# Performance work log

Hardware: AMD Instinct MI355X
Metric: run time of the kernel (lower is better)

Reference implementation:

```python
import jax, jax.numpy as jnp
import numpy as np

# dims (match init_kwargs)
N, M = 128, 2048
DX, DY, DU, DZ = 64, 8, 256, 256
EPS = 0.01


def setup_inputs() -> dict:
    key = jax.random.key(0)
    kit = iter(jax.random.split(key, 40))
    def w(*shape):
        fan_in = shape[-1]
        return jax.random.normal(next(kit), shape, jnp.float32) / np.float32(np.sqrt(fan_in))
    def b(*shape):
        return 0.1 * jax.random.normal(next(kit), shape, jnp.float32)
    inp = {
        'X_tensor': jax.random.normal(next(kit), (N, DX), jnp.float32),
        'U_tensor': jax.random.normal(next(kit), (M, DY), jnp.float32),
        'Y_tensor': jax.random.normal(next(kit), (N, DY), jnp.float32),
        # context path (x -> u_i)
        'Wt0': w(DU, DX), 'bt0': b(DU),
        'Wt1': w(DU, DU), 'bt1': b(DU),
        # PICNN cell 0 (input cell, no z term)
        'Wyu0': w(DY, DX), 'byu0': b(DY), 'Wy0': w(DZ, DY), 'Wu0': w(DZ, DX), 'b0': b(DZ),
        # PICNN cell 1 (hidden cell, nonneg Wz1 via softplus)
        'Wzu1': w(DZ, DU), 'bzu1': b(DZ), 'Wz1': w(DZ, DZ),
        'Wyu1': w(DY, DU), 'byu1': b(DY), 'Wy1': w(DZ, DY), 'Wu1': w(DZ, DU), 'b1': b(DZ),
        # PICNN cell 2 (output cell, scalar potential)
        'Wzu2': w(DZ, DU), 'bzu2': b(DZ), 'Wz2': w(1, DZ),
        'Wyu2': w(DY, DU), 'byu2': b(DY), 'Wy2': w(1, DY), 'Wu2': w(1, DU), 'b2': b(1),
    }
    return inp


def _psi(X, U, Y, Wt0, bt0, Wt1, bt1, Wyu0, byu0, Wy0, Wu0, b0,
         Wzu1, bzu1, Wz1, Wyu1, byu1, Wy1, Wu1, b1,
         Wzu2, bzu2, Wz2, Wyu2, byu2, Wy2, Wu2, b2):
    relu = jax.nn.relu
    # context path depends only on X -> compute once per row, broadcast over m samples
    u1 = relu(X @ Wt0.T + bt0)                       # [n, du]
    u2 = relu(u1 @ Wt1.T + bt1)                      # [n, du]
    # cell 0: z1 [n, m, dz]  (pairwise over X rows x U samples)
    gy0 = X @ Wyu0.T + byu0                          # [n, dy]
    z1 = relu(jnp.einsum('md,nd,zd->nmz', U, gy0, Wy0)
              + (X @ Wu0.T + b0)[:, None, :])
    # cell 1: hidden convex cell with nonneg z-weight
    gz1 = relu(u1 @ Wzu1.T + bzu1)                   # [n, dz]
    gy1 = u1 @ Wyu1.T + byu1                         # [n, dy]
    z2 = relu(jnp.einsum('nmz,nz,kz->nmk', z1, gz1, jax.nn.softplus(Wz1))
              + jnp.einsum('md,nd,kd->nmk', U, gy1, Wy1)
              + (u1 @ Wu1.T + b1)[:, None, :])       # [n, m, dz]
    # output cell -> scalar potential phi(x_i, u_j)
    gz2 = relu(u2 @ Wzu2.T + bzu2)                   # [n, dz]
    gy2 = u2 @ Wyu2.T + byu2                         # [n, dy]
    phi = (jnp.einsum('nmz,nz,z->nm', z2, gz2, jax.nn.softplus(Wz2)[0])
           + jnp.einsum('md,nd,d->nm', U, gy2, Wy2[0])
           + (u2 @ Wu2[0] + b2[0])[:, None])         # [n, m]
    # entropic OT dual psi with stable row-wise logsumexp
    cost = Y @ U.T                                   # [n, m]
    slack = cost - phi
    row_max = jnp.max(slack, axis=1, keepdims=True)
    log_mean_exp = (jax.nn.logsumexp((slack - row_max) / EPS, axis=1, keepdims=True)
                    - jnp.log(jnp.float32(slack.shape[1])))
    return EPS * (log_mean_exp + row_max / EPS)      # [n, 1]


def reference(X_tensor, U_tensor, Y_tensor, Wt0, bt0, Wt1, bt1, Wyu0, byu0, Wy0, Wu0, b0,
              Wzu1, bzu1, Wz1, Wyu1, byu1, Wy1, Wu1, b1,
              Wzu2, bzu2, Wz2, Wyu2, byu2, Wy2, Wu2, b2):
    return _psi(X_tensor, U_tensor, Y_tensor, Wt0, bt0, Wt1, bt1, Wyu0, byu0, Wy0, Wu0, b0,
                Wzu1, bzu1, Wz1, Wyu1, byu1, Wy1, Wu1, b1,
                Wzu2, bzu2, Wz2, Wyu2, byu2, Wy2, Wu2, b2)
```

## Files before the change

### kernel.cpp

```cpp
#include <hip/hip_runtime.h>

#define NN 128
#define MM 2048
#define EPSF 0.01f

typedef __bf16 bf16x8 __attribute__((ext_vector_type(8)));
typedef __bf16 bf16x4 __attribute__((ext_vector_type(4)));
typedef float  f32x4  __attribute__((ext_vector_type(4)));

#define WS_SLACK 0
#define WS_W2    262144
#define WS_GZ1   294912
#define WS_YV    327680
#define WS_CU2   328704
#define WS_WTB   328832
#define WS_A2    361600
#define WS_B2    394368
#define WS_BX    918656
#define WS_U1    1442944
#define WS_U2    1459328
#define WS_C0    1475712
#define WS_C1    1492096
#define WS_GY0   1508480
#define WS_GY1   1509504

__device__ __forceinline__ float softplusf(float x) {
    return x > 20.f ? x : log1pf(expf(x));
}

__device__ __forceinline__ bf16x8 ld_cvt8(const float* __restrict__ p) {
    const float4* p4 = (const float4*)p;
    float4 a = p4[0], b = p4[1];
    bf16x8 r;
    r[0] = (__bf16)a.x; r[1] = (__bf16)a.y; r[2] = (__bf16)a.z; r[3] = (__bf16)a.w;
    r[4] = (__bf16)b.x; r[5] = (__bf16)b.y; r[6] = (__bf16)b.z; r[7] = (__bf16)b.w;
    return r;
}


__global__ __launch_bounds__(256) void k_l1(
    const float* __restrict__ X,
    const float* __restrict__ Wt0, const float* __restrict__ bt0,
    const float* __restrict__ Wu0, const float* __restrict__ b0,
    const float* __restrict__ Wyu0, const float* __restrict__ byu0,
    float* __restrict__ ws)
{
    const int t = threadIdx.x, w = t >> 6, lane = t & 63;
    const int c = lane & 15, q = lane >> 4;
    const int nb = blockIdx.y * 16;
    const int ct = blockIdx.x * 4 + w;
    if (ct >= 33) return;

    bf16x8 a1[2];
#pragma unroll
    for (int ch = 0; ch < 2; ++ch)
        a1[ch] = ld_cvt8(X + (nb + c) * 64 + ch * 32 + q * 8);

    const float* rp;
    int col;
    if (ct < 16)      { col = ct * 16 + c;        rp = Wt0 + col * 64; }
    else if (ct < 32) { col = (ct - 16) * 16 + c; rp = Wu0 + col * 64; }
    else              { col = c & 7;              rp = Wyu0 + col * 64; }

    f32x4 D = {0.f, 0.f, 0.f, 0.f};
#pragma unroll
    for (int ch = 0; ch < 2; ++ch) {
        bf16x8 b = ld_cvt8(rp + ch * 32 + q * 8);
        D = __builtin_amdgcn_mfma_f32_16x16x32_bf16(a1[ch], b, D, 0, 0, 0);
    }

    if (ct < 16) {
        __bf16* u1p = (__bf16*)(ws + WS_U1);
        const float bv = bt0[col];
#pragma unroll
        for (int r = 0; r < 4; ++r)
            u1p[(nb + 4 * q + r) * 256 + col] = (__bf16)fmaxf(D[r] + bv, 0.f);
    } else if (ct < 32) {
        __bf16* c0p = (__bf16*)(ws + WS_C0);
        const float bv = b0[col];
#pragma unroll
        for (int r = 0; r < 4; ++r)
            c0p[(nb + 4 * q + r) * 256 + col] = (__bf16)(D[r] + bv);
    } else if (c < 8) {
        const float bv = byu0[c];
#pragma unroll
        for (int r = 0; r < 4; ++r)
            ws[WS_GY0 + (nb + 4 * q + r) * 8 + c] = D[r] + bv;
    }
}

__global__ __launch_bounds__(256) void k_l2(
    const float* __restrict__ Wt1, const float* __restrict__ bt1,
    const float* __restrict__ Wzu1, const float* __restrict__ bzu1,
    const float* __restrict__ Wu1, const float* __restrict__ b1,
    const float* __restrict__ Wyu1, const float* __restrict__ byu1,
    float* __restrict__ ws)
{
    const int t = threadIdx.x, w = t >> 6, lane = t & 63;
    const int c = lane & 15, q = lane >> 4;
    const int nb = blockIdx.y * 16;
    const int ct = blockIdx.x * 4 + w;
    if (ct >= 49) return;

    const __bf16* u1p = (const __bf16*)(ws + WS_U1);
    bf16x8 aF[8];
#pragma unroll
    for (int ch = 0; ch < 8; ++ch)
        aF[ch] = *(const bf16x8*)(u1p + (nb + c) * 256 + ch * 32 + q * 8);

    const float* rp;
    int col;
    if (ct < 16)      { col = ct * 16 + c;        rp = Wt1 + col * 256; }
    else if (ct < 32) { col = (ct - 16) * 16 + c; rp = Wzu1 + col * 256; }
    else if (ct < 48) { col = (ct - 32) * 16 + c; rp = Wu1 + col * 256; }
    else              { col = c & 7;              rp = Wyu1 + col * 256; }

    f32x4 D = {0.f, 0.f, 0.f, 0.f};
#pragma unroll
    for (int ch = 0; ch < 8; ++ch) {
        bf16x8 b = ld_cvt8(rp + ch * 32 + q * 8);
        D = __builtin_amdgcn_mfma_f32_16x16x32_bf16(aF[ch], b, D, 0, 0, 0);
    }

    if (ct < 16) {
        __bf16* u2p = (__bf16*)(ws + WS_U2);
        const float bv = bt1[col];
#pragma unroll
        for (int r = 0; r < 4; ++r)
            u2p[(nb + 4 * q + r) * 256 + col] = (__bf16)fmaxf(D[r] + bv, 0.f);
    } else if (ct < 32) {
        const float bv = bzu1[col];
#pragma unroll
        for (int r = 0; r < 4; ++r)
            ws[WS_GZ1 + (nb + 4 * q + r) * 256 + col] = fmaxf(D[r] + bv, 0.f);
    } else if (ct < 48) {
        __bf16* c1p = (__bf16*)(ws + WS_C1);
        const float bv = b1[col];
#pragma unroll
        for (int r = 0; r < 4; ++r)
            c1p[(nb + 4 * q + r) * 256 + col] = (__bf16)(D[r] + bv);
    } else if (c < 8) {
        const float bv = byu1[c];
#pragma unroll
        for (int r = 0; r < 4; ++r)
            ws[WS_GY1 + (nb + 4 * q + r) * 8 + c] = D[r] + bv;
    }
}

__global__ __launch_bounds__(256) void k_l3(
    const float* __restrict__ Y,
    const float* __restrict__ Wzu2, const float* __restrict__ bzu2,
    const float* __restrict__ Wz2,
    const float* __restrict__ Wyu2, const float* __restrict__ byu2,
    const float* __restrict__ Wy2,
    const float* __restrict__ Wu2, const float* __restrict__ b2,
    float* __restrict__ ws)
{
    const int t = threadIdx.x, w = t >> 6, lane = t & 63;
    const int c = lane & 15, q = lane >> 4;
    const int nb = blockIdx.y * 16;
    const int ct = blockIdx.x * 4 + w;
    if (ct >= 17) return;

    const __bf16* u2p = (const __bf16*)(ws + WS_U2);
    bf16x8 aF[8];
#pragma unroll
    for (int ch = 0; ch < 8; ++ch)
        aF[ch] = *(const bf16x8*)(u2p + (nb + c) * 256 + ch * 32 + q * 8);

    const float* rp;
    int col = 0;
    if (ct < 16) { col = ct * 16 + c; rp = Wzu2 + col * 256; }
    else         { rp = (c < 8) ? (Wyu2 + c * 256) : Wu2; }

    f32x4 D = {0.f, 0.f, 0.f, 0.f};
#pragma unroll
    for (int ch = 0; ch < 8; ++ch) {
        bf16x8 b = ld_cvt8(rp + ch * 32 + q * 8);
        D = __builtin_amdgcn_mfma_f32_16x16x32_bf16(aF[ch], b, D, 0, 0, 0);
    }

    if (ct < 16) {
        const float bv = bzu2[col];
        const float sp = softplusf(Wz2[col]);
#pragma unroll
        for (int r = 0; r < 4; ++r) {
            float gz2 = fmaxf(D[r] + bv, 0.f);
            ws[WS_W2 + (nb + 4 * q + r) * 256 + col] = gz2 * sp;
        }
    } else if (c < 8) {
        const float bv = byu2[c];
        const float wy2 = Wy2[c];
#pragma unroll
        for (int r = 0; r < 4; ++r) {
            const int n = nb + 4 * q + r;
            ws[WS_YV + n * 8 + c] = Y[n * 8 + c] - (D[r] + bv) * wy2;
        }
    } else if (c == 8) {
#pragma unroll
        for (int r = 0; r < 4; ++r)
            ws[WS_CU2 + nb + 4 * q + r] = D[r] + b2[0];
    }
}

__global__ __launch_bounds__(256) void k_bmat(
    const float* __restrict__ Wz1, const float* __restrict__ U,
    const float* __restrict__ Wy0, const float* __restrict__ Wy1,
    float* __restrict__ ws)
{
    const int b = blockIdx.x, t = threadIdx.x;
    const int i = b * 256 + t;

    ((__bf16*)(ws + WS_WTB))[i] = (__bf16)softplusf(Wz1[i]);
    {
        int m = i >> 5, cc = i & 31;
        float v = cc < 8 ? U[m * 8 + cc] : (cc == 8 ? 1.f : 0.f);
        ((__bf16*)(ws + WS_A2))[i] = (__bf16)v;
    }

    const int which = b >> 7, n = b & 127, z = t;
    const float* wy = (which ? Wy1 : Wy0) + z * 8;
    const float* gy = ws + (which ? WS_GY1 : WS_GY0) + n * 8;
    const __bf16* cp = (const __bf16*)(ws + (which ? WS_C1 : WS_C0)) + n * 256 + z;
    __bf16* dst = (__bf16*)(ws + (which ? WS_BX : WS_B2)) + (n * 256 + z) * 32;

    bf16x8 zz;
#pragma unroll
    for (int j = 0; j < 8; ++j) zz[j] = (__bf16)0.f;
    bf16x8 v0, v1 = zz;
#pragma unroll
    for (int d = 0; d < 8; ++d) v0[d] = (__bf16)(gy[d] * wy[d]);
    v1[0] = *cp;
    *(bf16x8*)(dst)      = v0;
    *(bf16x8*)(dst + 8)  = v1;
    *(bf16x8*)(dst + 16) = zz;
    *(bf16x8*)(dst + 24) = zz;
}

__global__ __launch_bounds__(256, 4) void k_main(
    const float* __restrict__ U,
    float* __restrict__ ws)
{
    __shared__ __bf16 zh[64][264];
    __shared__ float gz1s[256];
    __shared__ float w2s[256];
    __shared__ float sdot[64];
    __shared__ float psum[4][64];

    const int t  = threadIdx.x;
    const int n  = blockIdx.y;
    const int m0 = blockIdx.x * 64;
    const int w    = t >> 6;
    const int lane = t & 63;
    const int c = lane & 15;
    const int q = lane >> 4;

    gz1s[t] = ws[WS_GZ1 + n * 256 + t];
    w2s[t]  = ws[WS_W2  + n * 256 + t];
    if (t < 64) {
        float sd = 0.f;
#pragma unroll
        for (int d = 0; d < 8; ++d)
            sd += U[(m0 + t) * 8 + d] * ws[WS_YV + n * 8 + d];
        sdot[t] = sd;
    }

    const __bf16* A2p = (const __bf16*)(ws + WS_A2);
    const __bf16* B2p = (const __bf16*)(ws + WS_B2) + n * 8192;
    const __bf16* BXp = (const __bf16*)(ws + WS_BX) + n * 8192;
    const __bf16* WTp = (const __bf16*)(ws + WS_WTB);

    bf16x8 a2f[4];
#pragma unroll
    for (int mi = 0; mi < 4; ++mi)
        a2f[mi] = *(const bf16x8*)(A2p + (m0 + 16 * mi + c) * 32 + q * 8);

    {
        bf16x8 b2f[4];
#pragma unroll
        for (int zt = 0; zt < 4; ++zt)
            b2f[zt] = *(const bf16x8*)(B2p + (64 * w + 16 * zt + c) * 32 + q * 8);
        f32x4 pre[4][4];
#pragma unroll
        for (int zt = 0; zt < 4; ++zt)
#pragma unroll
            for (int mi = 0; mi < 4; ++mi) {
                f32x4 zacc = {0.f, 0.f, 0.f, 0.f};
                pre[zt][mi] = __builtin_amdgcn_mfma_f32_16x16x32_bf16(
                    b2f[zt], a2f[mi], zacc, 0, 0, 0);
            }
#pragma unroll
        for (int zt = 0; zt < 4; ++zt) {
            const int zb = 64 * w + 16 * zt + 4 * q;
#pragma unroll
            for (int mi = 0; mi < 4; ++mi) {
                bf16x4 v4;
#pragma unroll
                for (int r = 0; r < 4; ++r)
                    v4[r] = (__bf16)(fmaxf(pre[zt][mi][r], 0.f) * gz1s[zb + r]);
                *(bf16x4*)&zh[c + 16 * mi][zb] = v4;
            }
        }
    }

    f32x4 acc[4][4];
#pragma unroll
    for (int mi = 0; mi < 4; ++mi)
#pragma unroll
        for (int kj = 0; kj < 4; ++kj)
            acc[mi][kj] = f32x4{0.f, 0.f, 0.f, 0.f};

    __syncthreads();

    for (int ch = 0; ch < 8; ++ch) {
        bf16x8 az[4], bw[4];
#pragma unroll
        for (int mi = 0; mi < 4; ++mi)
            az[mi] = *(const bf16x8*)&zh[c + 16 * mi][ch * 32 + q * 8];
#pragma unroll
        for (int kj = 0; kj < 4; ++kj)
            bw[kj] = *(const bf16x8*)(WTp + (64 * w + 16 * kj + c) * 256 + ch * 32 + q * 8);
#pragma unroll
        for (int mi = 0; mi < 4; ++mi)
#pragma unroll
            for (int kj = 0; kj < 4; ++kj)
                acc[mi][kj] = __builtin_amdgcn_mfma_f32_16x16x32_bf16(
                    az[mi], bw[kj], acc[mi][kj], 0, 0, 0);
    }
    {
        bf16x8 bx[4];
#pragma unroll
        for (int kj = 0; kj < 4; ++kj)
            bx[kj] = *(const bf16x8*)(BXp + (64 * w + 16 * kj + c) * 32 + q * 8);
#pragma unroll
        for (int mi = 0; mi < 4; ++mi)
#pragma unroll
            for (int kj = 0; kj < 4; ++kj)
                acc[mi][kj] = __builtin_amdgcn_mfma_f32_16x16x32_bf16(
                    a2f[mi], bx[kj], acc[mi][kj], 0, 0, 0);
    }

    float p[4][4];
#pragma unroll
    for (int mi = 0; mi < 4; ++mi)
#pragma unroll
        for (int r = 0; r < 4; ++r) p[mi][r] = 0.f;
#pragma unroll
    for (int kj = 0; kj < 4; ++kj) {
        float w2v = w2s[64 * w + 16 * kj + c];
#pragma unroll
        for (int mi = 0; mi < 4; ++mi)
#pragma unroll
            for (int r = 0; r < 4; ++r)
                p[mi][r] += fmaxf(acc[mi][kj][r], 0.f) * w2v;
    }
#pragma unroll
    for (int mi = 0; mi < 4; ++mi)
#pragma unroll
        for (int r = 0; r < 4; ++r) {
            float v = p[mi][r];
            v += __shfl_xor(v, 8);
            v += __shfl_xor(v, 4);
            v += __shfl_xor(v, 2);
            v += __shfl_xor(v, 1);
            p[mi][r] = v;
        }
    if (c == 0) {
#pragma unroll
        for (int mi = 0; mi < 4; ++mi)
            *(float4*)&psum[w][16 * mi + 4 * q] =
                make_float4(p[mi][0], p[mi][1], p[mi][2], p[mi][3]);
    }
    __syncthreads();
    if (t < 64) {
        float cu2 = ws[WS_CU2 + n];
        float pp = psum[0][t] + psum[1][t] + psum[2][t] + psum[3][t];
        ws[WS_SLACK + n * 2048 + m0 + t] = sdot[t] - cu2 - pp;
    }
}

__global__ __launch_bounds__(256) void k_lse(const float* __restrict__ ws,
                                             float* __restrict__ out) {
    __shared__ float redmax[4];
    __shared__ float redsum[4];
    const int n = blockIdx.x;
    const int t = threadIdx.x;
    const float* s = ws + WS_SLACK + n * 2048;

    float vals[8];
    float mx = -3.4e38f;
#pragma unroll
    for (int i = 0; i < 8; ++i) {
        vals[i] = s[t + 256 * i];
        mx = fmaxf(mx, vals[i]);
    }
#pragma unroll
    for (int off = 32; off; off >>= 1) mx = fmaxf(mx, __shfl_xor(mx, off));
    if ((t & 63) == 0) redmax[t >> 6] = mx;
    __syncthreads();
    mx = fmaxf(fmaxf(redmax[0], redmax[1]), fmaxf(redmax[2], redmax[3]));

    float sum = 0.f;
#pragma unroll
    for (int i = 0; i < 8; ++i) sum += expf((vals[i] - mx) * (1.f / EPSF));
#pragma unroll
    for (int off = 32; off; off >>= 1) sum += __shfl_xor(sum, off);
    if ((t & 63) == 0) redsum[t >> 6] = sum;
    __syncthreads();
    if (t == 0) {
        float S = redsum[0] + redsum[1] + redsum[2] + redsum[3];
        out[n] = EPSF * logf(S * (1.f / 2048.f)) + mx;
    }
}

extern "C" void kernel_launch(void* const* d_in, const int* in_sizes, int n_in,
                              void* d_out, int out_size, void* d_ws, size_t ws_size,
                              hipStream_t stream) {
    const float* X    = (const float*)d_in[0];
    const float* Uu   = (const float*)d_in[1];
    const float* Yy   = (const float*)d_in[2];
    const float* Wt0  = (const float*)d_in[3];
    const float* bt0  = (const float*)d_in[4];
    const float* Wt1  = (const float*)d_in[5];
    const float* bt1  = (const float*)d_in[6];
    const float* Wyu0 = (const float*)d_in[7];
    const float* byu0 = (const float*)d_in[8];
    const float* Wy0  = (const float*)d_in[9];
    const float* Wu0  = (const float*)d_in[10];
    const float* b0   = (const float*)d_in[11];
    const float* Wzu1 = (const float*)d_in[12];
    const float* bzu1 = (const float*)d_in[13];
    const float* Wz1  = (const float*)d_in[14];
    const float* Wyu1 = (const float*)d_in[15];
    const float* byu1 = (const float*)d_in[16];
    const float* Wy1  = (const float*)d_in[17];
    const float* Wu1  = (const float*)d_in[18];
    const float* b1   = (const float*)d_in[19];
    const float* Wzu2 = (const float*)d_in[20];
    const float* bzu2 = (const float*)d_in[21];
    const float* Wz2  = (const float*)d_in[22];
    const float* Wyu2 = (const float*)d_in[23];
    const float* byu2 = (const float*)d_in[24];
    const float* Wy2  = (const float*)d_in[25];
    const float* Wu2  = (const float*)d_in[26];
    const float* b2   = (const float*)d_in[27];
    float* ws  = (float*)d_ws;
    float* out = (float*)d_out;

    k_l1<<<dim3(9, 8),  dim3(256), 0, stream>>>(X, Wt0, bt0, Wu0, b0, Wyu0, byu0, ws);
    k_l2<<<dim3(13, 8), dim3(256), 0, stream>>>(Wt1, bt1, Wzu1, bzu1, Wu1, b1, Wyu1, byu1, ws);
    k_l3<<<dim3(5, 8),  dim3(256), 0, stream>>>(Yy, Wzu2, bzu2, Wz2, Wyu2, byu2, Wy2, Wu2, b2, ws);
    k_bmat<<<dim3(256), dim3(256), 0, stream>>>(Wz1, Uu, Wy0, Wy1, ws);
    k_main<<<dim3(MM / 64, NN), dim3(256), 0, stream>>>(Uu, ws);
    k_lse<<<dim3(128), dim3(256), 0, stream>>>(ws, out);
}
```

Baseline: 203.6 us.

## Eliminate k_bmat by building MFMA operands in-register inside main kernel

Removes the separate k_bmat kernel that materialized padded bf16 A2/B2/BX operand tensors in the workspace. The softplus(Wz1) conversion moves into extra blocks of the first layer kernel. The main kernel now builds the U and Wy·gy operand fragments directly from U, Wy0/Wy1, gy and c vectors in registers. It also double-buffers the Wz1 weight-fragment loads across the K loop and lowers the occupancy hint from 4 to 3 blocks. This saves one launch and a large workspace write/read, at the cost of more register pressure and some redundant per-block operand construction.

```diff
diff --git a/kernel.cpp b/kernel.cpp
--- a/kernel.cpp
+++ b/kernel.cpp
@@ -14,15 +14,12 @@
 #define WS_YV    327680
 #define WS_CU2   328704
 #define WS_WTB   328832
-#define WS_A2    361600
-#define WS_B2    394368
-#define WS_BX    918656
-#define WS_U1    1442944
-#define WS_U2    1459328
-#define WS_C0    1475712
-#define WS_C1    1492096
-#define WS_GY0   1508480
-#define WS_GY1   1509504
+#define WS_U1    361600
+#define WS_U2    377984
+#define WS_C0    394368
+#define WS_C1    410752
+#define WS_GY0   427136
+#define WS_GY1   428160
 
 __device__ __forceinline__ float softplusf(float x) {
     return x > 20.f ? x : log1pf(expf(x));
@@ -37,18 +34,29 @@
     return r;
 }
 
-
-__global__ __launch_bounds__(256) void k_l1(
+__global__ __launch_bounds__(256) void k_s1(
     const float* __restrict__ X,
     const float* __restrict__ Wt0, const float* __restrict__ bt0,
     const float* __restrict__ Wu0, const float* __restrict__ b0,
     const float* __restrict__ Wyu0, const float* __restrict__ byu0,
+    const float* __restrict__ Wz1,
     float* __restrict__ ws)
 {
-    const int t = threadIdx.x, w = t >> 6, lane = t & 63;
+    const int t = threadIdx.x, bx = blockIdx.x;
+    if (bx >= 9) {
+        if (blockIdx.y != 0) return;
+        const int i = (bx - 9) * 1024 + t * 4;
+        float4 v = *(const float4*)(Wz1 + i);
+        bf16x4 r;
+        r[0] = (__bf16)softplusf(v.x); r[1] = (__bf16)softplusf(v.y);
+        r[2] = (__bf16)softplusf(v.z); r[3] = (__bf16)softplusf(v.w);
+        *(bf16x4*)((__bf16*)(ws + WS_WTB) + i) = r;
+        return;
+    }
+    const int w = t >> 6, lane = t & 63;
     const int c = lane & 15, q = lane >> 4;
     const int nb = blockIdx.y * 16;
-    const int ct = blockIdx.x * 4 + w;
+    const int ct = bx * 4 + w;
     if (ct >= 33) return;
 
     bf16x8 a1[2];
@@ -89,7 +97,7 @@
     }
 }
 
-__global__ __launch_bounds__(256) void k_l2(
+__global__ __launch_bounds__(256) void k_s2(
     const float* __restrict__ Wt1, const float* __restrict__ bt1,
     const float* __restrict__ Wzu1, const float* __restrict__ bzu1,
     const float* __restrict__ Wu1, const float* __restrict__ b1,
@@ -147,7 +155,7 @@
     }
 }
 
-__global__ __launch_bounds__(256) void k_l3(
+__global__ __launch_bounds__(256) void k_s3(
     const float* __restrict__ Y,
     const float* __restrict__ Wzu2, const float* __restrict__ bzu2,
     const float* __restrict__ Wz2,
@@ -203,42 +211,10 @@
     }
 }
 
-__global__ __launch_bounds__(256) void k_bmat(
-    const float* __restrict__ Wz1, const float* __restrict__ U,
-    const float* __restrict__ Wy0, const float* __restrict__ Wy1,
-    float* __restrict__ ws)
-{
-    const int b = blockIdx.x, t = threadIdx.x;
-    const int i = b * 256 + t;
-
-    ((__bf16*)(ws + WS_WTB))[i] = (__bf16)softplusf(Wz1[i]);
-    {
-        int m = i >> 5, cc = i & 31;
-        float v = cc < 8 ? U[m * 8 + cc] : (cc == 8 ? 1.f : 0.f);
-        ((__bf16*)(ws + WS_A2))[i] = (__bf16)v;
-    }
-
-    const int which = b >> 7, n = b & 127, z = t;
-    const float* wy = (which ? Wy1 : Wy0) + z * 8;
-    const float* gy = ws + (which ? WS_GY1 : WS_GY0) + n * 8;
-    const __bf16* cp = (const __bf16*)(ws + (which ? WS_C1 : WS_C0)) + n * 256 + z;
-    __bf16* dst = (__bf16*)(ws + (which ? WS_BX : WS_B2)) + (n * 256 + z) * 32;
-
-    bf16x8 zz;
-#pragma unroll
-    for (int j = 0; j < 8; ++j) zz[j] = (__bf16)0.f;
-    bf16x8 v0, v1 = zz;
-#pragma unroll
-    for (int d = 0; d < 8; ++d) v0[d] = (__bf16)(gy[d] * wy[d]);
-    v1[0] = *cp;
-    *(bf16x8*)(dst)      = v0;
-    *(bf16x8*)(dst + 8)  = v1;
-    *(bf16x8*)(dst + 16) = zz;
-    *(bf16x8*)(dst + 24) = zz;
-}
-
-__global__ __launch_bounds__(256, 4) void k_main(
+__global__ __launch_bounds__(256, 3) void k_main(
     const float* __restrict__ U,
+    const float* __restrict__ Wy0,
+    const float* __restrict__ Wy1,
     float* __restrict__ ws)
 {
     __shared__ __bf16 zh[64][264];
@@ -265,41 +241,59 @@
         sdot[t] = sd;
     }
 
-    const __bf16* A2p = (const __bf16*)(ws + WS_A2);
-    const __bf16* B2p = (const __bf16*)(ws + WS_B2) + n * 8192;
-    const __bf16* BXp = (const __bf16*)(ws + WS_BX) + n * 8192;
+    const __bf16* c0p = (const __bf16*)(ws + WS_C0) + n * 256;
+    const __bf16* c1p = (const __bf16*)(ws + WS_C1) + n * 256;
     const __bf16* WTp = (const __bf16*)(ws + WS_WTB);
 
+    float g0[8], g1[8];
+    {
+        const float4* p0 = (const float4*)(ws + WS_GY0 + n * 8);
+        const float4* p1 = (const float4*)(ws + WS_GY1 + n * 8);
+        float4 a = p0[0], b = p0[1];
+        g0[0]=a.x; g0[1]=a.y; g0[2]=a.z; g0[3]=a.w; g0[4]=b.x; g0[5]=b.y; g0[6]=b.z; g0[7]=b.w;
+        a = p1[0]; b = p1[1];
+        g1[0]=a.x; g1[1]=a.y; g1[2]=a.z; g1[3]=a.w; g1[4]=b.x; g1[5]=b.y; g1[6]=b.z; g1[7]=b.w;
+    }
+
     bf16x8 a2f[4];
 #pragma unroll
-    for (int mi = 0; mi < 4; ++mi)
-        a2f[mi] = *(const bf16x8*)(A2p + (m0 + 16 * mi + c) * 32 + q * 8);
-
-    {
-        bf16x8 b2f[4];
-#pragma unroll
-        for (int zt = 0; zt < 4; ++zt)
-            b2f[zt] = *(const bf16x8*)(B2p + (64 * w + 16 * zt + c) * 32 + q * 8);
-        f32x4 pre[4][4];
-#pragma unroll
-        for (int zt = 0; zt < 4; ++zt)
-#pragma unroll
-            for (int mi = 0; mi < 4; ++mi) {
-                f32x4 zacc = {0.f, 0.f, 0.f, 0.f};
-                pre[zt][mi] = __builtin_amdgcn_mfma_f32_16x16x32_bf16(
-                    b2f[zt], a2f[mi], zacc, 0, 0, 0);
-            }
-#pragma unroll
-        for (int zt = 0; zt < 4; ++zt) {
-            const int zb = 64 * w + 16 * zt + 4 * q;
-#pragma unroll
-            for (int mi = 0; mi < 4; ++mi) {
-                bf16x4 v4;
-#pragma unroll
-                for (int r = 0; r < 4; ++r)
-                    v4[r] = (__bf16)(fmaxf(pre[zt][mi][r], 0.f) * gz1s[zb + r]);
-                *(bf16x4*)&zh[c + 16 * mi][zb] = v4;
-            }
+    for (int mi = 0; mi < 4; ++mi) {
+        const float4* up = (const float4*)(U + (m0 + c + 16 * mi) * 8);
+        float4 u0 = up[0], u1 = up[1];
+        float uv[8] = {u0.x, u0.y, u0.z, u0.w, u1.x, u1.y, u1.z, u1.w};
+#pragma unroll
+        for (int j = 0; j < 8; ++j)
+            a2f[mi][j] = (q == 0) ? (__bf16)uv[j] : (__bf16)0.f;
+        if (q == 1) a2f[mi][0] = (__bf16)1.f;
+    }
+
+#pragma unroll
+    for (int zt = 0; zt < 4; ++zt) {
+        const int z = 64 * w + 16 * zt + c;
+        const float4* wy = (const float4*)(Wy0 + z * 8);
+        float4 wa = wy[0], wb = wy[1];
+        float wv[8] = {wa.x, wa.y, wa.z, wa.w, wb.x, wb.y, wb.z, wb.w};
+        const float c0v = (float)c0p[z];
+        bf16x8 b2f;
+#pragma unroll
+        for (int j = 0; j < 8; ++j)
+            b2f[j] = (q == 0) ? (__bf16)(g0[j] * wv[j]) : (__bf16)0.f;
+        if (q == 1) b2f[0] = (__bf16)c0v;
+
+        f32x4 pr[4];
+#pragma unroll
+        for (int mi = 0; mi < 4; ++mi) {
+            f32x4 zacc = {0.f, 0.f, 0.f, 0.f};
+            pr[mi] = __builtin_amdgcn_mfma_f32_16x16x32_bf16(b2f, a2f[mi], zacc, 0, 0, 0);
+        }
+        const int zb = 64 * w + 16 * zt + 4 * q;
+#pragma unroll
+        for (int mi = 0; mi < 4; ++mi) {
+            bf16x4 v4;
+#pragma unroll
+            for (int r = 0; r < 4; ++r)
+                v4[r] = (__bf16)(fmaxf(pr[mi][r], 0.f) * gz1s[zb + r]);
+            *(bf16x4*)&zh[c + 16 * mi][zb] = v4;
         }
     }
 
@@ -312,32 +306,49 @@
 
     __syncthreads();
 
+    bf16x8 bwA[4], bwB[4];
+#pragma unroll
+    for (int kj = 0; kj < 4; ++kj)
+        bwA[kj] = *(const bf16x8*)(WTp + (64 * w + 16 * kj + c) * 256 + q * 8);
+
+#pragma unroll
     for (int ch = 0; ch < 8; ++ch) {
-        bf16x8 az[4], bw[4];
+        bf16x8* curb = (ch & 1) ? bwB : bwA;
+        bf16x8* nxtb = (ch & 1) ? bwA : bwB;
+        if (ch < 7) {
+#pragma unroll
+            for (int kj = 0; kj < 4; ++kj)
+                nxtb[kj] = *(const bf16x8*)(WTp + (64 * w + 16 * kj + c) * 256 +
+                                            (ch + 1) * 32 + q * 8);
+        }
+        bf16x8 az[4];
 #pragma unroll
         for (int mi = 0; mi < 4; ++mi)
             az[mi] = *(const bf16x8*)&zh[c + 16 * mi][ch * 32 + q * 8];
 #pragma unroll
-        for (int kj = 0; kj < 4; ++kj)
-            bw[kj] = *(const bf16x8*)(WTp + (64 * w + 16 * kj + c) * 256 + ch * 32 + q * 8);
-#pragma unroll
         for (int mi = 0; mi < 4; ++mi)
 #pragma unroll
             for (int kj = 0; kj < 4; ++kj)
                 acc[mi][kj] = __builtin_amdgcn_mfma_f32_16x16x32_bf16(
-                    az[mi], bw[kj], acc[mi][kj], 0, 0, 0);
-    }
-    {
-        bf16x8 bx[4];
-#pragma unroll
-        for (int kj = 0; kj < 4; ++kj)
-            bx[kj] = *(const bf16x8*)(BXp + (64 * w + 16 * kj + c) * 32 + q * 8);
+                    az[mi], curb[kj], acc[mi][kj], 0, 0, 0);
+    }
+
+#pragma unroll
+    for (int kj = 0; kj < 4; ++kj) {
+        const int k = 64 * w + 16 * kj + c;
+        const float4* wy = (const float4*)(Wy1 + k * 8);
+        float4 wa = wy[0], wb = wy[1];
+        float wv[8] = {wa.x, wa.y, wa.z, wa.w, wb.x, wb.y, wb.z, wb.w};
+        const float c1v = (float)c1p[k];
+        bf16x8 bx;
+#pragma unroll
+        for (int j = 0; j < 8; ++j)
+            bx[j] = (q == 0) ? (__bf16)(g1[j] * wv[j]) : (__bf16)0.f;
+        if (q == 1) bx[0] = (__bf16)c1v;
 #pragma unroll
         for (int mi = 0; mi < 4; ++mi)
-#pragma unroll
-            for (int kj = 0; kj < 4; ++kj)
-                acc[mi][kj] = __builtin_amdgcn_mfma_f32_16x16x32_bf16(
-                    a2f[mi], bx[kj], acc[mi][kj], 0, 0, 0);
+            acc[mi][kj] = __builtin_amdgcn_mfma_f32_16x16x32_bf16(
+                a2f[mi], bx, acc[mi][kj], 0, 0, 0);
     }
 
     float p[4][4];
@@ -447,10 +458,9 @@
     float* ws  = (float*)d_ws;
     float* out = (float*)d_out;
 
-    k_l1<<<dim3(9, 8),  dim3(256), 0, stream>>>(X, Wt0, bt0, Wu0, b0, Wyu0, byu0, ws);
-    k_l2<<<dim3(13, 8), dim3(256), 0, stream>>>(Wt1, bt1, Wzu1, bzu1, Wu1, b1, Wyu1, byu1, ws);
-    k_l3<<<dim3(5, 8),  dim3(256), 0, stream>>>(Yy, Wzu2, bzu2, Wz2, Wyu2, byu2, Wy2, Wu2, b2, ws);
-    k_bmat<<<dim3(256), dim3(256), 0, stream>>>(Wz1, Uu, Wy0, Wy1, ws);
-    k_main<<<dim3(MM / 64, NN), dim3(256), 0, stream>>>(Uu, ws);
+    k_s1<<<dim3(73, 8),  dim3(256), 0, stream>>>(X, Wt0, bt0, Wu0, b0, Wyu0, byu0, Wz1, ws);
+    k_s2<<<dim3(13, 8), dim3(256), 0, stream>>>(Wt1, bt1, Wzu1, bzu1, Wu1, b1, Wyu1, byu1, ws);
+    k_s3<<<dim3(5, 8),  dim3(256), 0, stream>>>(Yy, Wzu2, bzu2, Wz2, Wyu2, byu2, Wy2, Wu2, b2, ws);
+    k_main<<<dim3(MM / 64, NN), dim3(256), 0, stream>>>(Uu, Wy0, Wy1, ws);
     k_lse<<<dim3(128), dim3(256), 0, stream>>>(ws, out);
 }
```

Measured after the change: 217.1 us. +6.7%, slower.
